# Kernel optimization log

Hardware: AMD Instinct MI355X
Metric: run time of the kernel (lower is better)

The kernel has to match this reference:

```python
import jax, jax.numpy as jnp
import numpy as np

# YOLOv5-style NMS + scale_coords constants
CONF_THRES = 0.25
IOU_THRES = 0.45
MAX_DET = 300      # max detections kept per image
TOPK = 1024        # candidate pool fed to greedy NMS (static for jit)
MAX_WH = 4096.0    # class offset for class-aware NMS
IMG1 = (640.0, 640.0)   # shape1: letterboxed network input (h, w)
IMG0 = (720.0, 1280.0)  # shape0: original image (h, w)


def xywh2xyxy(x):
    xy, wh = x[..., :2], x[..., 2:4] * 0.5
    return jnp.concatenate([xy - wh, xy + wh], axis=-1)


def iou_one_to_many(b, B):
    # b: [4], B: [K,4] in xyxy
    lt = jnp.maximum(b[:2], B[:, :2])
    rb = jnp.minimum(b[2:], B[:, 2:])
    wh = jnp.clip(rb - lt, 0.0)
    inter = wh[:, 0] * wh[:, 1]
    a1 = (b[2] - b[0]) * (b[3] - b[1])
    a2 = (B[:, 2] - B[:, 0]) * (B[:, 3] - B[:, 1])
    return inter / (a1 + a2 - inter + 1e-9)


def nms_single(pred):
    # pred: [N, 85] = xywh, obj, 80 class scores
    obj = pred[:, 4]
    conf_all = obj[:, None] * pred[:, 5:]          # obj * cls conf
    conf = conf_all.max(axis=-1)
    cls = jnp.argmax(conf_all, axis=-1).astype(pred.dtype)
    boxes = xywh2xyxy(pred[:, :4])
    valid = (obj > CONF_THRES) & (conf > CONF_THRES)
    sc = jnp.where(valid, conf, -1.0)
    sc_top, idx = jax.lax.top_k(sc, TOPK)          # candidate pool
    b = boxes[idx]                                  # [K,4]
    c = cls[idx]                                    # [K]
    off = b + c[:, None] * MAX_WH                   # class-aware offset boxes

    def body(i, state):
        s, sel, selv = state
        p = jnp.argmax(s)
        pv = s[p] > 0.0
        iou = iou_one_to_many(off[p], off)
        s = jnp.where(iou > IOU_THRES, -1.0, s).at[p].set(-1.0)
        return s, sel.at[i].set(p), selv.at[i].set(pv)

    init = (sc_top, jnp.zeros(MAX_DET, jnp.int32), jnp.zeros(MAX_DET, bool))
    _, sel, selv = jax.lax.fori_loop(0, MAX_DET, body, init)

    det = jnp.concatenate(
        [b[sel], sc_top[sel][:, None], c[sel][:, None]], axis=-1)  # [max_det,6]
    return jnp.where(selv[:, None], det, 0.0)


def scale_coords(coords):
    # undo letterbox: IMG1 (h1,w1) -> IMG0 (h0,w0)
    h1, w1 = IMG1
    h0, w0 = IMG0
    gain = min(h1 / h0, w1 / w0)
    pad_x = (w1 - w0 * gain) / 2.0
    pad_y = (h1 - h0 * gain) / 2.0
    x1 = jnp.clip((coords[..., 0] - pad_x) / gain, 0.0, w0)
    y1 = jnp.clip((coords[..., 1] - pad_y) / gain, 0.0, h0)
    x2 = jnp.clip((coords[..., 2] - pad_x) / gain, 0.0, w0)
    y2 = jnp.clip((coords[..., 3] - pad_y) / gain, 0.0, h0)
    return jnp.stack([x1, y1, x2, y2], axis=-1)


def setup_inputs() -> dict:
    key = jax.random.key(0)
    kxy, kwh, kobj, kcls = jax.random.split(key, 4)
    B, N, NC = 16, 25200, 80
    xy = jax.random.uniform(kxy, (B, N, 2), jnp.float32) * 640.0
    wh = jax.random.uniform(kwh, (B, N, 2), jnp.float32) * 160.0 + 2.0
    obj = jax.random.uniform(kobj, (B, N, 1), jnp.float32)
    cls = jax.random.uniform(kcls, (B, N, NC), jnp.float32)
    pred = jnp.concatenate([xy, wh, obj, cls], axis=-1)  # [B, N, 85]
    return {"pred": pred}


def reference(pred):
    det = jax.vmap(nms_single)(pred)                 # [B, max_det, 6]
    boxes = scale_coords(det[..., :4])
    # columns: x1,y1,x2,y2 (rescaled), score, label
    return jnp.concatenate([boxes, det[..., 4:]], axis=-1)
```

## Files before the change

### kernel.cpp

```cpp
#include <hip/hip_runtime.h>
#include <stdint.h>

#define N_CAND 25200
#define NB 16
#define ROW 85
#define TK 1024
#define MAXDET 300
#define CAP 2048
#define BITS_LO 0x3E800000u
#define TRI_WORDS 7680

typedef unsigned long long u64;
typedef unsigned int u32;

static __device__ __forceinline__ u64 u64min(u64 a, u64 b) { return a < b ? a : b; }
static __device__ __forceinline__ u64 u64max(u64 a, u64 b) { return a > b ? a : b; }
static __device__ __forceinline__ int triBase(int w) { return 64 * (15 * w - (w * (w - 1)) / 2); }

__global__ __launch_bounds__(256, 8) void score_kernel(const float* __restrict__ pred,
                                                       u64* __restrict__ keys)
{
#pragma clang fp contract(off)
    __shared__ float tile[64 * ROW];
    const int tid = threadIdx.x;
    const int row0 = blockIdx.x * 64;
    const float4* src = (const float4*)(pred + (size_t)row0 * ROW);
    float4* dst = (float4*)tile;
#pragma unroll
    for (int i = 0; i < 6; ++i) {
        int idx = tid + (i << 8);
        if (idx < (64 * ROW) / 4) {
            __builtin_amdgcn_global_load_lds(
                (const __attribute__((address_space(1))) void*)(src + idx),
                (__attribute__((address_space(3))) void*)(dst + idx),
                16, 0, 0);
        }
    }
    __syncthreads();

    const int r = tid >> 2, sub = tid & 3;
    const float* rowp = tile + r * ROW;
    const float obj = rowp[4];
    const int base = 5 + sub * 20;
    float bv = obj * rowp[base];
    int bi = base - 5;
#pragma unroll
    for (int c = 1; c < 20; ++c) {
        float p = obj * rowp[base + c];
        if (p > bv) { bv = p; bi = base - 5 + c; }
    }
#pragma unroll
    for (int off = 1; off <= 2; off <<= 1) {
        float ov = __shfl_xor(bv, off, 64);
        int   oi = __shfl_xor(bi, off, 64);
        if (ov > bv || (ov == bv && oi < bi)) { bv = ov; bi = oi; }
    }
    if (sub == 0) {
        int w = row0 + r;
        u32 n = (u32)w % N_CAND;
        u64 key = 0;
        if (obj > 0.25f && bv > 0.25f)
            key = ((u64)__float_as_uint(bv) << 32) | (((u64)(25199u - n)) << 7) | (u32)bi;
        keys[w] = key;
    }
}

__global__ __launch_bounds__(1024) void topk_kernel(const float* __restrict__ pred,
                                                    const u64* __restrict__ keys,
                                                    float4* __restrict__ soaA,
                                                    float4* __restrict__ soaB)
{
#pragma clang fp contract(off)
    __shared__ u64 sbuf[CAP];
    __shared__ u32 histA[2048];
    __shared__ u32 histB[2048];
    __shared__ u32 s_t;
    __shared__ int s_fb;

    const int tid = threadIdx.x;
    const int b = blockIdx.x;
    const u64* kb = keys + (size_t)b * N_CAND;
    const float* pb = pred + (size_t)b * N_CAND * ROW;

    for (int i = tid; i < 2048; i += 1024) histA[i] = 0;
    for (int i = tid; i < CAP; i += 1024) sbuf[i] = 0ull;
    if (tid == 0) { s_t = 0; s_fb = 0; }
    __syncthreads();

    for (int n = tid; n < N_CAND; n += 1024) {
        u32 bits = (u32)(kb[n] >> 32);
        if (bits) {
            int bin = (int)((bits - BITS_LO) >> 13);
            bin = bin < 0 ? 0 : (bin > 2047 ? 2047 : bin);
            atomicAdd(&histA[bin], 1u);
        }
    }
    __syncthreads();

    u32* srcp = histA; u32* dstp = histB;
    for (int step = 1; step < 2048; step <<= 1) {
        for (int i = tid; i < 2048; i += 1024)
            dstp[i] = srcp[i] + ((i + step < 2048) ? srcp[i + step] : 0u);
        __syncthreads();
        u32* t = srcp; srcp = dstp; dstp = t;
    }
    for (int i = tid; i < 2048; i += 1024) {
        u32 S = srcp[i];
        if (S >= TK && (i == 2047 || srcp[i + 1] < TK)) s_t = (u32)i;
    }
    __syncthreads();
    const int t = (int)s_t;
    const u32 thr = BITS_LO + ((u32)t << 13);

    for (int i = tid; i < 2048; i += 1024) {
        u32 base = (i < 2047) ? srcp[i + 1] : 0u;
        dstp[i] = base;
        if (i >= t && (srcp[i] - base) > 64u) s_fb = 1;
    }
    __syncthreads();

    for (int n = tid; n < N_CAND; n += 1024) {
        u64 k = kb[n];
        u32 bits = (u32)(k >> 32);
        if (bits >= thr) {
            int bin = (int)((bits - BITS_LO) >> 13);
            bin = bin < 0 ? 0 : (bin > 2047 ? 2047 : bin);
            u32 pos = atomicAdd(&dstp[bin], 1u);
            if (pos < CAP) sbuf[pos] = k;
        }
    }
    __syncthreads();

    if (!s_fb) {
        const int wave = tid >> 6, lane = tid & 63;
        for (int bin = t + wave; bin < 2048; bin += 16) {
            u32 base = (bin < 2047) ? srcp[bin + 1] : 0u;
            u32 end = srcp[bin]; if (end > CAP) end = CAP;
            if (end <= base + 1) continue;
            u32 cnt_b = end - base;
            u64 v = (lane < (int)cnt_b) ? sbuf[base + lane] : 0ull;
#pragma unroll
            for (int k2 = 2; k2 <= 64; k2 <<= 1) {
                for (int j = k2 >> 1; j > 0; j >>= 1) {
                    u64 p = __shfl_xor(v, j, 64);
                    const bool up = ((lane & k2) == 0);
                    const bool low = ((lane & j) == 0);
                    v = (up == low) ? u64max(v, p) : u64min(v, p);
                }
            }
            if (lane < (int)cnt_b) sbuf[base + lane] = v;
        }
        __syncthreads();
    } else {
        const int E0 = tid << 1;
        u64 e0 = sbuf[E0], e1 = sbuf[E0 + 1];
        for (int k = 2; k <= CAP; k <<= 1) {
            for (int j = k >> 1; j > 0; j >>= 1) {
                const bool asc = ((E0 & k) == 0);
                if (j >= 128) {
                    __syncthreads();
                    sbuf[E0] = e0; sbuf[E0 + 1] = e1;
                    __syncthreads();
                    u64 p0 = sbuf[E0 ^ j], p1 = sbuf[(E0 + 1) ^ j];
                    const bool low = ((E0 & j) == 0);
                    e0 = (asc == low) ? u64min(e0, p0) : u64max(e0, p0);
                    e1 = (asc == low) ? u64min(e1, p1) : u64max(e1, p1);
                } else if (j >= 2) {
                    const int l = j >> 1;
                    u64 p0 = __shfl_xor(e0, l, 64);
                    u64 p1 = __shfl_xor(e1, l, 64);
                    const bool low = ((E0 & j) == 0);
                    e0 = (asc == low) ? u64min(e0, p0) : u64max(e0, p0);
                    e1 = (asc == low) ? u64min(e1, p1) : u64max(e1, p1);
                } else {
                    u64 mn = u64min(e0, e1), mx = u64max(e0, e1);
                    e0 = asc ? mn : mx;
                    e1 = asc ? mx : mn;
                }
            }
        }
        __syncthreads();
        sbuf[E0] = e0; sbuf[E0 + 1] = e1;
        __syncthreads();
    }

    {
        const int i = tid;
        u64 k = sbuf[s_fb ? (CAP - 1 - i) : i];
        u32 bits = (u32)(k >> 32);
        float4 A, Bv;
        if (bits) {
            u32 lo = (u32)k;
            u32 n = 25199u - (lo >> 7);
            float c = (float)(lo & 127u);
            const float* rp = pb + (size_t)n * ROW;
            float x = rp[0], y = rp[1], ww = rp[2], hh = rp[3];
            float hw = ww * 0.5f, hv = hh * 0.5f;
            float x1 = x - hw, y1 = y - hv, x2 = x + hw, y2 = y + hv;
            float offc = c * 4096.0f;
            float area = ((x2 + offc) - (x1 + offc)) * ((y2 + offc) - (y1 + offc));
            A = make_float4(x1, y1, x2, y2);
            Bv = make_float4(area, __uint_as_float(bits), c, 0.0f);
        } else {
            A = make_float4(0.0f, 0.0f, 0.0f, 0.0f);
            Bv = make_float4(0.0f, -1.0f, 0.0f, 0.0f);
        }
        soaA[b * TK + i] = A;
        soaB[b * TK + i] = Bv;
    }
}

__global__ __launch_bounds__(512) void mask_kernel(const float4* __restrict__ soaA,
                                                   const float4* __restrict__ soaB,
                                                   u64* __restrict__ tri,
                                                   u64* __restrict__ diagArr)
{
#pragma clang fp contract(off)
    __shared__ float qx1[TK], qy1[TK], qx2[TK], qy2[TK], qar[TK];
    const int tid = threadIdx.x;
    const int b = blockIdx.y;
    const int rbase = blockIdx.x * 32;
    const int wi = rbase >> 6;
    for (int i = tid; i < TK; i += 512) {
        float4 A = soaA[b * TK + i];
        float4 Bv = soaB[b * TK + i];
        float off = Bv.z * 4096.0f;
        qx1[i] = A.x + off; qy1[i] = A.y + off;
        qx2[i] = A.z + off; qy2[i] = A.w + off;
        qar[i] = Bv.x;
    }
    __syncthreads();

    u64* trib = tri + (size_t)b * TRI_WORDS;
    const int Bw = triBase(wi);
    const int s = 15 - wi;

    const int wave = tid >> 6, lane = tid & 63;
    for (int rr = 0; rr < 4; ++rr) {
        int i = rbase + (wave << 2) + rr;
        int r = i & 63;
        float px1 = qx1[i], py1 = qy1[i];
        float px2 = qx2[i], py2 = qy2[i];
        float parea = qar[i];
        u64 myword = 0;
        for (int word = wi; word < 16; ++word) {
            int j = (word << 6) + lane;
            float ltx = fmaxf(px1, qx1[j]), lty = fmaxf(py1, qy1[j]);
            float rbx = fminf(px2, qx2[j]), rby = fminf(py2, qy2[j]);
            float w2 = fmaxf(rbx - ltx, 0.0f), h2 = fmaxf(rby - lty, 0.0f);
            float inter = w2 * h2;
            float iou = inter / (parea + qar[j] - inter + 1e-9f);
            u64 m = __ballot(iou > 0.45f);
            if (lane == word) myword = m;
        }
        if (lane == wi) diagArr[(b << 10) + i] = myword;
        else if (lane > wi && lane < 16) trib[Bw + r * s + (lane - wi - 1)] = myword;
    }
}

__global__ __launch_bounds__(1024) void sweep_kernel(const float4* __restrict__ soaA,
                                                     const float4* __restrict__ soaB,
                                                     const u64* __restrict__ tri,
                                                     const u64* __restrict__ diagArr,
                                                     float* __restrict__ out)
{
#pragma clang fp contract(off)
    __shared__ u64 tri_lds[TRI_WORDS];
    __shared__ int sel[MAXDET];
    __shared__ int s_nsel;
    const int tid = threadIdx.x;
    const int b = blockIdx.x;

    const u64* gtri = tri + (size_t)b * TRI_WORDS;
    for (int i = tid; i < TRI_WORDS; i += 1024) tri_lds[i] = gtri[i];
    __syncthreads();

    if (tid < 64) {
        const int lane = tid;
        const u64* db = diagArr + (b << 10);

        int nv = TK;
        for (int k = 0; k < 16; ++k) {
            float s = soaB[b * TK + (k << 6) + lane].y;
            u64 m = __ballot(s > 0.0f);
            if (m != ~0ull) { nv = (k << 6) + (int)__builtin_ctzll(~m); break; }
        }

        u64 removed = 0;
        int nsel = 0;
        const int g = lane >> 4;
        const int word = lane & 15;
        u64 diag = db[lane];
        for (int w = 0; w < 16; ++w) {
            u64 dnext = (w < 15) ? db[((w + 1) << 6) + lane] : 0ull;
            u64 wv = __shfl(removed, w, 64);
            int rem = nv - (w << 6);
            u64 validm = (rem >= 64) ? ~0ull : ((rem <= 0) ? 0ull : ((1ull << rem) - 1ull));
            u64 alive = validm & ~wv;
            u64 selbits = 0;
            while (alive != 0ull && nsel < MAXDET) {
                int i = (int)__builtin_ctzll(alive);
                if (lane == 0) sel[nsel] = (w << 6) + i;
                ++nsel;
                selbits |= (1ull << i);
                u64 d = __shfl(diag, i, 64);
                alive &= ~d;
                alive &= ~(1ull << i);
            }
            if (selbits != 0ull && w < 15) {
                const int Bw = triBase(w);
                const int s = 15 - w;
                u64 sb = selbits;
                if (g >= 1 && sb) sb &= sb - 1;
                if (g >= 2 && sb) sb &= sb - 1;
                if (g >= 3 && sb) sb &= sb - 1;
                u64 acc = 0;
                while (sb) {
                    int i = (int)__builtin_ctzll(sb);
                    if (word > w) acc |= tri_lds[Bw + i * s + (word - w - 1)];
                    sb &= sb - 1; if (sb) { sb &= sb - 1; if (sb) { sb &= sb - 1; if (sb) sb &= sb - 1; } }
                }
                acc |= __shfl_xor(acc, 16, 64);
                acc |= __shfl_xor(acc, 32, 64);
                removed |= acc;
            }
            diag = dnext;
            if (nsel >= MAXDET || rem <= 64) break;
        }
        if (lane == 0) s_nsel = nsel;
    }
    __syncthreads();

    const int nsel = s_nsel;
    for (int r = tid; r < MAXDET; r += 1024) {
        float* o = out + ((size_t)b * MAXDET + r) * 6;
        if (r < nsel) {
            int p = sel[r];
            float4 A = soaA[b * TK + p];
            float4 Bv = soaB[b * TK + p];
            float X1 = (A.x - 0.0f) / 0.5f;
            float Y1 = (A.y - 140.0f) / 0.5f;
            float X2 = (A.z - 0.0f) / 0.5f;
            float Y2 = (A.w - 140.0f) / 0.5f;
            X1 = fminf(fmaxf(X1, 0.0f), 1280.0f);
            Y1 = fminf(fmaxf(Y1, 0.0f), 720.0f);
            X2 = fminf(fmaxf(X2, 0.0f), 1280.0f);
            Y2 = fminf(fmaxf(Y2, 0.0f), 720.0f);
            o[0] = X1; o[1] = Y1; o[2] = X2; o[3] = Y2;
            o[4] = Bv.y; o[5] = Bv.z;
        } else {
            o[0] = 0.0f; o[1] = 0.0f; o[2] = 0.0f;
            o[3] = 0.0f; o[4] = 0.0f; o[5] = 0.0f;
        }
    }
}

extern "C" void kernel_launch(void* const* d_in, const int* in_sizes, int n_in,
                              void* d_out, int out_size, void* d_ws, size_t ws_size,
                              hipStream_t stream)
{
    const float* pred = (const float*)d_in[0];
    float* out = (float*)d_out;

    u64* keys = (u64*)d_ws;
    u64* tri = (u64*)d_ws;
    u64* diagArr = (u64*)((char*)d_ws + 983040);
    float4* soaA = (float4*)((char*)d_ws + 3225600);
    float4* soaB = (float4*)((char*)d_ws + 3225600 + 262144);

    score_kernel<<<(NB * N_CAND) / 64, 256, 0, stream>>>(pred, keys);
    topk_kernel<<<NB, 1024, 0, stream>>>(pred, keys, soaA, soaB);
    mask_kernel<<<dim3(32, NB), 512, 0, stream>>>(soaA, soaB, tri, diagArr);
    sweep_kernel<<<NB, 1024, 0, stream>>>(soaA, soaB, tri, diagArr, out);
}
```

Measured before the change: 126.4 us.

## Store full row-major NMS masks in padded LDS and cache top-k keys in registers

The packed triangular IoU mask and separate diagonal array are replaced by a full 16-word mask per candidate. The sweep kernel stages this into LDS with a padded stride of 17 words and reads both the diagonal and the suppression words from there, which removes the triangular index arithmetic and the prefetch from global memory. Separately, top-k now loads each thread's 25 keys into registers once, so the histogram pass and the scatter pass no longer both read them from global memory. The costs are roughly twice the IoU work in the mask kernel, more mask data to write and load, about 139 KB of LDS for the sweep block, and 25 extra 64-bit registers per thread in top-k.

```diff
diff --git a/kernel.cpp b/kernel.cpp
--- a/kernel.cpp
+++ b/kernel.cpp
@@ -8,14 +8,14 @@
 #define MAXDET 300
 #define CAP 2048
 #define BITS_LO 0x3E800000u
-#define TRI_WORDS 7680
+#define KPT 25
+#define LDW 17
 
 typedef unsigned long long u64;
 typedef unsigned int u32;
 
 static __device__ __forceinline__ u64 u64min(u64 a, u64 b) { return a < b ? a : b; }
 static __device__ __forceinline__ u64 u64max(u64 a, u64 b) { return a > b ? a : b; }
-static __device__ __forceinline__ int triBase(int w) { return 64 * (15 * w - (w * (w - 1)) / 2); }
 
 __global__ __launch_bounds__(256, 8) void score_kernel(const float* __restrict__ pred,
                                                        u64* __restrict__ keys)
@@ -82,13 +82,21 @@
     const u64* kb = keys + (size_t)b * N_CAND;
     const float* pb = pred + (size_t)b * N_CAND * ROW;
 
+    u64 rk[KPT];
+#pragma unroll
+    for (int s = 0; s < KPT; ++s) {
+        int n = tid + (s << 10);
+        rk[s] = (n < N_CAND) ? kb[n] : 0ull;
+    }
+
     for (int i = tid; i < 2048; i += 1024) histA[i] = 0;
     for (int i = tid; i < CAP; i += 1024) sbuf[i] = 0ull;
     if (tid == 0) { s_t = 0; s_fb = 0; }
     __syncthreads();
 
-    for (int n = tid; n < N_CAND; n += 1024) {
-        u32 bits = (u32)(kb[n] >> 32);
+#pragma unroll
+    for (int s = 0; s < KPT; ++s) {
+        u32 bits = (u32)(rk[s] >> 32);
         if (bits) {
             int bin = (int)((bits - BITS_LO) >> 13);
             bin = bin < 0 ? 0 : (bin > 2047 ? 2047 : bin);
@@ -119,8 +127,9 @@
     }
     __syncthreads();
 
-    for (int n = tid; n < N_CAND; n += 1024) {
-        u64 k = kb[n];
+#pragma unroll
+    for (int s = 0; s < KPT; ++s) {
+        u64 k = rk[s];
         u32 bits = (u32)(k >> 32);
         if (bits >= thr) {
             int bin = (int)((bits - BITS_LO) >> 13);
@@ -212,15 +221,13 @@
 
 __global__ __launch_bounds__(512) void mask_kernel(const float4* __restrict__ soaA,
                                                    const float4* __restrict__ soaB,
-                                                   u64* __restrict__ tri,
-                                                   u64* __restrict__ diagArr)
+                                                   u64* __restrict__ masks)
 {
 #pragma clang fp contract(off)
     __shared__ float qx1[TK], qy1[TK], qx2[TK], qy2[TK], qar[TK];
     const int tid = threadIdx.x;
     const int b = blockIdx.y;
     const int rbase = blockIdx.x * 32;
-    const int wi = rbase >> 6;
     for (int i = tid; i < TK; i += 512) {
         float4 A = soaA[b * TK + i];
         float4 Bv = soaB[b * TK + i];
@@ -231,19 +238,14 @@
     }
     __syncthreads();
 
-    u64* trib = tri + (size_t)b * TRI_WORDS;
-    const int Bw = triBase(wi);
-    const int s = 15 - wi;
-
     const int wave = tid >> 6, lane = tid & 63;
     for (int rr = 0; rr < 4; ++rr) {
         int i = rbase + (wave << 2) + rr;
-        int r = i & 63;
         float px1 = qx1[i], py1 = qy1[i];
         float px2 = qx2[i], py2 = qy2[i];
         float parea = qar[i];
         u64 myword = 0;
-        for (int word = wi; word < 16; ++word) {
+        for (int word = 0; word < 16; ++word) {
             int j = (word << 6) + lane;
             float ltx = fmaxf(px1, qx1[j]), lty = fmaxf(py1, qy1[j]);
             float rbx = fminf(px2, qx2[j]), rby = fminf(py2, qy2[j]);
@@ -253,31 +255,29 @@
             u64 m = __ballot(iou > 0.45f);
             if (lane == word) myword = m;
         }
-        if (lane == wi) diagArr[(b << 10) + i] = myword;
-        else if (lane > wi && lane < 16) trib[Bw + r * s + (lane - wi - 1)] = myword;
+        if (lane < 16) masks[((size_t)(b * TK + i) << 4) + lane] = myword;
     }
 }
 
 __global__ __launch_bounds__(1024) void sweep_kernel(const float4* __restrict__ soaA,
                                                      const float4* __restrict__ soaB,
-                                                     const u64* __restrict__ tri,
-                                                     const u64* __restrict__ diagArr,
+                                                     const u64* __restrict__ masks,
                                                      float* __restrict__ out)
 {
 #pragma clang fp contract(off)
-    __shared__ u64 tri_lds[TRI_WORDS];
+    __shared__ u64 fm[TK * LDW];
     __shared__ int sel[MAXDET];
     __shared__ int s_nsel;
     const int tid = threadIdx.x;
     const int b = blockIdx.x;
 
-    const u64* gtri = tri + (size_t)b * TRI_WORDS;
-    for (int i = tid; i < TRI_WORDS; i += 1024) tri_lds[i] = gtri[i];
+    const u64* gm = masks + ((size_t)(b * TK) << 4);
+    for (int idx = tid; idx < TK * 16; idx += 1024)
+        fm[(idx >> 4) * LDW + (idx & 15)] = gm[idx];
     __syncthreads();
 
     if (tid < 64) {
         const int lane = tid;
-        const u64* db = diagArr + (b << 10);
 
         int nv = TK;
         for (int k = 0; k < 16; ++k) {
@@ -290,9 +290,8 @@
         int nsel = 0;
         const int g = lane >> 4;
         const int word = lane & 15;
-        u64 diag = db[lane];
         for (int w = 0; w < 16; ++w) {
-            u64 dnext = (w < 15) ? db[((w + 1) << 6) + lane] : 0ull;
+            u64 diag = fm[((w << 6) + lane) * LDW + w];
             u64 wv = __shfl(removed, w, 64);
             int rem = nv - (w << 6);
             u64 validm = (rem >= 64) ? ~0ull : ((rem <= 0) ? 0ull : ((1ull << rem) - 1ull));
@@ -308,8 +307,6 @@
                 alive &= ~(1ull << i);
             }
             if (selbits != 0ull && w < 15) {
-                const int Bw = triBase(w);
-                const int s = 15 - w;
                 u64 sb = selbits;
                 if (g >= 1 && sb) sb &= sb - 1;
                 if (g >= 2 && sb) sb &= sb - 1;
@@ -317,14 +314,13 @@
                 u64 acc = 0;
                 while (sb) {
                     int i = (int)__builtin_ctzll(sb);
-                    if (word > w) acc |= tri_lds[Bw + i * s + (word - w - 1)];
+                    acc |= fm[((w << 6) + i) * LDW + word];
                     sb &= sb - 1; if (sb) { sb &= sb - 1; if (sb) { sb &= sb - 1; if (sb) sb &= sb - 1; } }
                 }
                 acc |= __shfl_xor(acc, 16, 64);
                 acc |= __shfl_xor(acc, 32, 64);
                 removed |= acc;
             }
-            diag = dnext;
             if (nsel >= MAXDET || rem <= 64) break;
         }
         if (lane == 0) s_nsel = nsel;
@@ -363,13 +359,12 @@
     float* out = (float*)d_out;
 
     u64* keys = (u64*)d_ws;
-    u64* tri = (u64*)d_ws;
-    u64* diagArr = (u64*)((char*)d_ws + 983040);
+    u64* masks = (u64*)d_ws;
     float4* soaA = (float4*)((char*)d_ws + 3225600);
     float4* soaB = (float4*)((char*)d_ws + 3225600 + 262144);
 
     score_kernel<<<(NB * N_CAND) / 64, 256, 0, stream>>>(pred, keys);
     topk_kernel<<<NB, 1024, 0, stream>>>(pred, keys, soaA, soaB);
-    mask_kernel<<<dim3(32, NB), 512, 0, stream>>>(soaA, soaB, tri, diagArr);
-    sweep_kernel<<<NB, 1024, 0, stream>>>(soaA, soaB, tri, diagArr, out);
-}
+    mask_kernel<<<dim3(32, NB), 512, 0, stream>>>(soaA, soaB, masks);
+    sweep_kernel<<<NB, 1024, 0, stream>>>(soaA, soaB, masks, out);
+}
```

Measured after the change: 121.8 us. 1.04x faster.
